# Kernel tuning notes

Hardware: AMD Instinct MI355X
Metric: run time of the kernel (lower is better)

## Reference

```python
import jax, jax.numpy as jnp
import numpy as np


def setup_inputs() -> dict:
    key = jax.random.key(0)
    k1, k2 = jax.random.split(key)
    N, P1, P2, D = 2, 16384, 16384, 3
    cloud1 = jax.random.normal(k1, (N, P1, D), dtype=jnp.float32)
    cloud2 = jax.random.normal(k2, (N, P2, D), dtype=jnp.float32)
    return {"cloud1": cloud1, "cloud2": cloud2}


def reference(cloud1, cloud2):
    # Chamfer distance (tensorflow_graphics convention):
    #   mean_i min_j ||a_i - b_j||^2 + mean_j min_i ||a_i - b_j||^2, per batch.
    # Compute squared distances via the Gram trick to avoid a (N,P1,P2,3) tensor.
    sq1 = jnp.sum(cloud1 * cloud1, axis=-1)              # (N, P1)
    sq2 = jnp.sum(cloud2 * cloud2, axis=-1)              # (N, P2)
    inner = jnp.einsum("npd,nqd->npq", cloud1, cloud2)   # (N, P1, P2)
    sqdist = sq1[:, :, None] + sq2[:, None, :] - 2.0 * inner
    sqdist = jnp.maximum(sqdist, 0.0)  # numerical floor
    min_a_to_b = jnp.min(sqdist, axis=2)  # (N, P1)
    min_b_to_a = jnp.min(sqdist, axis=1)  # (N, P2)
    return jnp.mean(min_a_to_b, axis=1) + jnp.mean(min_b_to_a, axis=1)  # (N,)
```

## Files before the change

kernel.cpp:

```cpp
#include <hip/hip_runtime.h>

#define NBATCH 2
#define NPTS   16384
#define TPTS   32
#define NTILES (NPTS / TPTS)
#define JCH    8
#define NT_PER (NTILES / JCH)
#define TG     (NPTS / 256)

typedef float f32x16 __attribute__((ext_vector_type(16)));
typedef short s16x8  __attribute__((ext_vector_type(8)));

__device__ __forceinline__ unsigned short f2bf(float f) {
    unsigned u = __float_as_uint(f);
    u += 0x7FFF + ((u >> 16) & 1);
    return (unsigned short)(u >> 16);
}
__device__ __forceinline__ float bf2f(unsigned short h) {
    return __uint_as_float((unsigned)h << 16);
}

__device__ __forceinline__ f32x16 mfma32(s16x8 a, s16x8 b) {
    f32x16 d;
    asm volatile("v_mfma_f32_32x32x16_bf16 %0, %1, %2, 0"
                 : "=&v"(d) : "v"(a), "v"(b));
    return d;
}
__device__ __forceinline__ void min3f(float& acc, float x, float y) {
    asm("v_min3_f32 %0, %1, %2, %3" : "=v"(acc) : "v"(acc), "v"(x), "v"(y));
}
__device__ __forceinline__ float min3v(float x, float y, float z) {
    float r;
    asm("v_min3_f32 %0, %1, %2, %3" : "=v"(r) : "v"(x), "v"(y), "v"(z));
    return r;
}

__global__ __launch_bounds__(256) void pack_panels(
    const float* __restrict__ c1, const float* __restrict__ c2,
    unsigned short* __restrict__ apan, unsigned short* __restrict__ bpan,
    unsigned int* __restrict__ mins)
{
    int tid = blockIdx.x * 256 + threadIdx.x;
    if (tid < 2 * NBATCH * NPTS) mins[tid] = 0x7F7F7F7Fu;

    int lane   = tid & 63;
    int tile   = (tid >> 6) & (NTILES - 1);
    int n      = (tid >> 15) & 1;
    int whichB = (tid >> 16) & 1;
    int wc     = (tid >> 17) & 1;

    const float* src = wc ? c2 : c1;

    int p = tile * TPTS + (lane & 31);
    const float* q = src + ((size_t)n * NPTS + p) * 3;
    float x = q[0], y = q[1], z = q[2];

    unsigned short xh = f2bf(x), yh = f2bf(y), zh = f2bf(z);
    unsigned short xl = f2bf(x - bf2f(xh)), yl = f2bf(y - bf2f(yh)), zl = f2bf(z - bf2f(zh));
    float sq = x * x + y * y + z * z;
    unsigned short sh = f2bf(sq);
    unsigned short sl = f2bf(sq - bf2f(sh));
    const unsigned short one = 0x3F80;

    unsigned short slots[16];
    if (!whichB) {
        slots[0]=xh;  slots[1]=yh;  slots[2]=zh;
        slots[3]=xl;  slots[4]=yl;  slots[5]=zl;
        slots[6]=xh;  slots[7]=yh;  slots[8]=zh;
        slots[9]=one; slots[10]=one;
        slots[11]=sh; slots[12]=sl;
        slots[13]=0;  slots[14]=0;  slots[15]=0;
    } else {
        unsigned short mxh=f2bf(-2.f*bf2f(xh)), myh=f2bf(-2.f*bf2f(yh)), mzh=f2bf(-2.f*bf2f(zh));
        unsigned short mxl=f2bf(-2.f*bf2f(xl)), myl=f2bf(-2.f*bf2f(yl)), mzl=f2bf(-2.f*bf2f(zl));
        slots[0]=mxh; slots[1]=myh; slots[2]=mzh;
        slots[3]=mxh; slots[4]=myh; slots[5]=mzh;
        slots[6]=mxl; slots[7]=myl; slots[8]=mzl;
        slots[9]=sh;  slots[10]=sl;
        slots[11]=one; slots[12]=one;
        slots[13]=0;  slots[14]=0;  slots[15]=0;
    }

    int j0 = (lane >> 5) * 8;
    uint4 w;
    w.x = (unsigned)slots[j0+0] | ((unsigned)slots[j0+1] << 16);
    w.y = (unsigned)slots[j0+2] | ((unsigned)slots[j0+3] << 16);
    w.z = (unsigned)slots[j0+4] | ((unsigned)slots[j0+5] << 16);
    w.w = (unsigned)slots[j0+6] | ((unsigned)slots[j0+7] << 16);
    unsigned short* pan = whichB ? bpan : apan;
    uint4* dst = (uint4*)pan + ((size_t)((wc * 2 + n) * NTILES + tile) * 64 + lane);
    *dst = w;
}

__global__ __launch_bounds__(256, 4) void chamfer_rows(
    const unsigned short* __restrict__ apan, const unsigned short* __restrict__ bpan,
    unsigned int* __restrict__ mins )
{
    __shared__ float ldsr[128 * 33];

    int bid = blockIdx.x;
    const int jc  = bid & (JCH - 1); bid >>= 3;
    const int tg  = bid & (TG - 1);  bid >>= 6;
    const int n   = bid & 1;         bid >>= 1;
    const int dir = bid;

    const int lane   = threadIdx.x & 63;
    const int wv     = threadIdx.x >> 6;
    const int colw   = lane & 31;
    const int laneHi = lane >> 5;
    const int rt0    = tg * 8 + wv * 2;

    const s16x8 a0 = *(const s16x8*)(
        apan + ((size_t)((dir * 2 + n) * NTILES + rt0) * 64 + lane) * 8);
    const s16x8 a1 = *(const s16x8*)(
        apan + ((size_t)((dir * 2 + n) * NTILES + rt0 + 1) * 64 + lane) * 8);
    const unsigned short* B =
        bpan + ((size_t)(((1 - dir) * 2 + n) * NTILES + jc * NT_PER) * 64 + lane) * 8;

#define LDT(t) (*(const s16x8*)(B + (size_t)(t) * 512))

    float rm0[16], rm1[16];
    #pragma unroll
    for (int r = 0; r < 16; ++r) { rm0[r] = 3.0e38f; rm1[r] = 3.0e38f; }

    s16x8 b0 = LDT(0), b1 = LDT(1), b2 = LDT(2), b3 = LDT(3);

#define PHASE(bc0, bc1, p0, p1)                                               \
    {                                                                         \
        f32x16 dA = mfma32(a0, bc0);                                          \
        f32x16 dB = mfma32(a0, bc1);                                          \
        __builtin_amdgcn_sched_barrier(0);                                    \
        asm volatile("s_nop 7\n\ts_nop 7\n\ts_nop 7" :: "v"(dA), "v"(dB));    \
        __builtin_amdgcn_sched_barrier(0);                                    \
        _Pragma("unroll")                                                     \
        for (int r = 0; r < 16; ++r) min3f(rm0[r], dA[r], dB[r]);             \
        f32x16 dC = mfma32(a1, bc0);                                          \
        f32x16 dD = mfma32(a1, bc1);                                          \
        bc0 = LDT((p0) & (NT_PER - 1));                                       \
        bc1 = LDT((p1) & (NT_PER - 1));                                       \
        __builtin_amdgcn_sched_barrier(0);                                    \
        asm volatile("s_nop 7\n\ts_nop 7\n\ts_nop 7" :: "v"(dC), "v"(dD));    \
        __builtin_amdgcn_sched_barrier(0);                                    \
        _Pragma("unroll")                                                     \
        for (int r = 0; r < 16; ++r) min3f(rm1[r], dC[r], dD[r]);             \
    }

    #pragma unroll
    for (int tt = 0; tt < NT_PER / 4; ++tt) {
        PHASE(b0, b1, 4 * tt + 4, 4 * tt + 5);
        PHASE(b2, b3, 4 * tt + 6, 4 * tt + 7);
    }
#undef PHASE
#undef LDT

    unsigned int* md = mins + (size_t)(dir * NBATCH + n) * NPTS + tg * 256;
    const int tid = threadIdx.x;

    #pragma unroll
    for (int p = 0; p < 2; ++p) {
        const float* rm = p ? rm1 : rm0;
        #pragma unroll
        for (int r = 0; r < 16; ++r) {
            const int cr = (r & 3) + 8 * (r >> 2) + 4 * laneHi;
            ldsr[(wv * 32 + cr) * 33 + colw] = rm[r];
        }
        __syncthreads();
        if (tid < 128) {
            const float* Lr = &ldsr[tid * 33];
            float c = min3v(Lr[0], Lr[1], Lr[2]);
            #pragma unroll
            for (int u = 0; u < 14; ++u) c = min3v(c, Lr[3 + 2 * u], Lr[4 + 2 * u]);
            c = fminf(c, Lr[31]);
            int rowg = (tid >> 5) * 64 + p * 32 + (tid & 31);
            atomicMin(&md[rowg], __float_as_uint(fmaxf(c, 0.0f)));
        }
        __syncthreads();
    }
}

__global__ __launch_bounds__(1024) void chamfer_out(
    const unsigned int* __restrict__ mins, float* __restrict__ out)
{
    int n = blockIdx.x;
    float acc = 0.0f;
    for (int i = threadIdx.x; i < NPTS; i += 1024) {
        acc += __uint_as_float(mins[(0 * NBATCH + n) * NPTS + i]);
        acc += __uint_as_float(mins[(1 * NBATCH + n) * NPTS + i]);
    }
    for (int off = 32; off > 0; off >>= 1) acc += __shfl_down(acc, off, 64);
    __shared__ float sm[16];
    int wv = threadIdx.x >> 6, ln = threadIdx.x & 63;
    if (ln == 0) sm[wv] = acc;
    __syncthreads();
    if (threadIdx.x == 0) {
        float tot = 0.0f;
        #pragma unroll
        for (int w = 0; w < 16; ++w) tot += sm[w];
        out[n] = tot / (float)NPTS;
    }
}

extern "C" void kernel_launch(void* const* d_in, const int* in_sizes, int n_in,
                              void* d_out, int out_size, void* d_ws, size_t ws_size,
                              hipStream_t stream)
{
    const float* c1 = (const float*)d_in[0];
    const float* c2 = (const float*)d_in[1];
    float* out = (float*)d_out;

    char* ws = (char*)d_ws;
    unsigned int*   mins = (unsigned int*)ws;
    unsigned short* apan = (unsigned short*)(ws + (size_t)(2 * NBATCH * NPTS) * 4);
    unsigned short* bpan = apan + (size_t)2 * NBATCH * NTILES * 512;

    pack_panels<<<(1 << 18) / 256, 256, 0, stream>>>(c1, c2, apan, bpan, mins);
    chamfer_rows<<<2 * NBATCH * TG * JCH, 256, 0, stream>>>(apan, bpan, mins);
    chamfer_out<<<NBATCH, 1024, 0, stream>>>(mins, out);
}
```

Before: 52.15 us.

## Stage B tiles through double-buffered LDS shared across waves

```diff
diff --git a/kernel.cpp b/kernel.cpp
--- a/kernel.cpp
+++ b/kernel.cpp
@@ -6,6 +6,7 @@
 #define NTILES (NPTS / TPTS)
 #define JCH    8
 #define NT_PER (NTILES / JCH)
+#define NQUAD  (NT_PER / 4)
 #define TG     (NPTS / 256)
 
 typedef float f32x16 __attribute__((ext_vector_type(16)));
@@ -97,6 +98,7 @@
     unsigned int* __restrict__ mins )
 {
     __shared__ float ldsr[128 * 33];
+    short* bst = (short*)ldsr;
 
     int bid = blockIdx.x;
     const int jc  = bid & (JCH - 1); bid >>= 3;
@@ -117,41 +119,49 @@
     const unsigned short* B =
         bpan + ((size_t)(((1 - dir) * 2 + n) * NTILES + jc * NT_PER) * 64 + lane) * 8;
 
-#define LDT(t) (*(const s16x8*)(B + (size_t)(t) * 512))
-
     float rm0[16], rm1[16];
     #pragma unroll
     for (int r = 0; r < 16; ++r) { rm0[r] = 3.0e38f; rm1[r] = 3.0e38f; }
 
-    s16x8 b0 = LDT(0), b1 = LDT(1), b2 = LDT(2), b3 = LDT(3);
-
-#define PHASE(bc0, bc1, p0, p1)                                               \
+#define DUOF(aa, rmv, tt0, tt1)                                               \
     {                                                                         \
-        f32x16 dA = mfma32(a0, bc0);                                          \
-        f32x16 dB = mfma32(a0, bc1);                                          \
+        f32x16 dX = mfma32(aa, tt0);                                          \
+        f32x16 dY = mfma32(aa, tt1);                                          \
         __builtin_amdgcn_sched_barrier(0);                                    \
-        asm volatile("s_nop 7\n\ts_nop 7\n\ts_nop 7" :: "v"(dA), "v"(dB));    \
+        asm volatile("s_nop 7\n\ts_nop 7\n\ts_nop 7" :: "v"(dX), "v"(dY));    \
         __builtin_amdgcn_sched_barrier(0);                                    \
         _Pragma("unroll")                                                     \
-        for (int r = 0; r < 16; ++r) min3f(rm0[r], dA[r], dB[r]);             \
-        f32x16 dC = mfma32(a1, bc0);                                          \
-        f32x16 dD = mfma32(a1, bc1);                                          \
-        bc0 = LDT((p0) & (NT_PER - 1));                                       \
-        bc1 = LDT((p1) & (NT_PER - 1));                                       \
-        __builtin_amdgcn_sched_barrier(0);                                    \
-        asm volatile("s_nop 7\n\ts_nop 7\n\ts_nop 7" :: "v"(dC), "v"(dD));    \
-        __builtin_amdgcn_sched_barrier(0);                                    \
-        _Pragma("unroll")                                                     \
-        for (int r = 0; r < 16; ++r) min3f(rm1[r], dC[r], dD[r]);             \
-    }
-
-    #pragma unroll
-    for (int tt = 0; tt < NT_PER / 4; ++tt) {
-        PHASE(b0, b1, 4 * tt + 4, 4 * tt + 5);
-        PHASE(b2, b3, 4 * tt + 6, 4 * tt + 7);
-    }
-#undef PHASE
-#undef LDT
+        for (int r = 0; r < 16; ++r) min3f(rmv[r], dX[r], dY[r]);             \
+    }
+
+    {
+        s16x8 g0 = *(const s16x8*)(B + (size_t)wv * 512);
+        *(s16x8*)(bst + wv * 512 + lane * 8) = g0;
+    }
+
+    #pragma unroll 2
+    for (int q = 0; q < NQUAD; ++q) {
+        const int b = q & 1;
+        __syncthreads();
+
+        const int nq = (q + 1) & (NQUAD - 1);
+        const s16x8 g = *(const s16x8*)(B + (size_t)(nq * 4 + wv) * 512);
+
+        const short* tb = bst + b * 2048 + lane * 8;
+        s16x8 t0 = *(const s16x8*)(tb);
+        s16x8 t1 = *(const s16x8*)(tb + 512);
+        s16x8 t2 = *(const s16x8*)(tb + 1024);
+        s16x8 t3 = *(const s16x8*)(tb + 1536);
+        DUOF(a0, rm0, t0, t1);
+        DUOF(a1, rm1, t0, t1);
+        DUOF(a0, rm0, t2, t3);
+        DUOF(a1, rm1, t2, t3);
+
+        *(s16x8*)(bst + (b ^ 1) * 2048 + wv * 512 + lane * 8) = g;
+    }
+#undef DUOF
+
+    __syncthreads();
 
     unsigned int* md = mins + (size_t)(dir * NBATCH + n) * NPTS + tg * 256;
     const int tid = threadIdx.x;
```

Result: faster. 50.55 us (-3.1%).

## Compute distance matrix once and reduce both row and column minima

Applied to the files above, without the earlier changes.

```diff
diff --git a/kernel.cpp b/kernel.cpp
--- a/kernel.cpp
+++ b/kernel.cpp
@@ -4,9 +4,9 @@
 #define NPTS   16384
 #define TPTS   32
 #define NTILES (NPTS / TPTS)
-#define JCH    8
+#define JCH    16
 #define NT_PER (NTILES / JCH)
-#define TG     (NPTS / 256)
+#define TG     (NPTS / 128)
 
 typedef float f32x16 __attribute__((ext_vector_type(16)));
 typedef short s16x8  __attribute__((ext_vector_type(8)));
@@ -19,6 +19,7 @@
 __device__ __forceinline__ float bf2f(unsigned short h) {
     return __uint_as_float((unsigned)h << 16);
 }
+__device__ __forceinline__ unsigned umin2(unsigned a, unsigned b) { return a < b ? a : b; }
 
 __device__ __forceinline__ f32x16 mfma32(s16x8 a, s16x8 b) {
     f32x16 d;
@@ -34,6 +35,13 @@
     asm("v_min3_f32 %0, %1, %2, %3" : "=v"(r) : "v"(x), "v"(y), "v"(z));
     return r;
 }
+__device__ __forceinline__ float tree16(const f32x16& d) {
+    float c = min3v(d[0], d[1], d[2]);
+    c = min3v(c, d[3],  d[4]);  c = min3v(c, d[5],  d[6]);
+    c = min3v(c, d[7],  d[8]);  c = min3v(c, d[9],  d[10]);
+    c = min3v(c, d[11], d[12]); c = min3v(c, d[13], d[14]);
+    return fminf(c, d[15]);
+}
 
 __global__ __launch_bounds__(256) void pack_panels(
     const float* __restrict__ c1, const float* __restrict__ c2,
@@ -47,9 +55,8 @@
     int tile   = (tid >> 6) & (NTILES - 1);
     int n      = (tid >> 15) & 1;
     int whichB = (tid >> 16) & 1;
-    int wc     = (tid >> 17) & 1;
-
-    const float* src = wc ? c2 : c1;
+
+    const float* src = whichB ? c2 : c1;
 
     int p = tile * TPTS + (lane & 31);
     const float* q = src + ((size_t)n * NPTS + p) * 3;
@@ -88,93 +95,96 @@
     w.z = (unsigned)slots[j0+4] | ((unsigned)slots[j0+5] << 16);
     w.w = (unsigned)slots[j0+6] | ((unsigned)slots[j0+7] << 16);
     unsigned short* pan = whichB ? bpan : apan;
-    uint4* dst = (uint4*)pan + ((size_t)((wc * 2 + n) * NTILES + tile) * 64 + lane);
+    uint4* dst = (uint4*)pan + ((size_t)(n * NTILES + tile) * 64 + lane);
     *dst = w;
 }
 
-__global__ __launch_bounds__(256, 4) void chamfer_rows(
+__global__ __launch_bounds__(256, 4) void chamfer_mm(
     const unsigned short* __restrict__ apan, const unsigned short* __restrict__ bpan,
-    unsigned int* __restrict__ mins )
+    unsigned int* __restrict__ rowmins, unsigned int* __restrict__ colmins)
 {
     __shared__ float ldsr[128 * 33];
+    unsigned int (*lcol)[NT_PER * 32] =
+        (unsigned int (*)[NT_PER * 32])ldsr;
 
     int bid = blockIdx.x;
-    const int jc  = bid & (JCH - 1); bid >>= 3;
-    const int tg  = bid & (TG - 1);  bid >>= 6;
-    const int n   = bid & 1;         bid >>= 1;
-    const int dir = bid;
+    const int jc = bid & (JCH - 1); bid >>= 4;
+    const int tg = bid & (TG - 1);  bid >>= 7;
+    const int n  = bid;
 
     const int lane   = threadIdx.x & 63;
     const int wv     = threadIdx.x >> 6;
     const int colw   = lane & 31;
     const int laneHi = lane >> 5;
-    const int rt0    = tg * 8 + wv * 2;
-
-    const s16x8 a0 = *(const s16x8*)(
-        apan + ((size_t)((dir * 2 + n) * NTILES + rt0) * 64 + lane) * 8);
-    const s16x8 a1 = *(const s16x8*)(
-        apan + ((size_t)((dir * 2 + n) * NTILES + rt0 + 1) * 64 + lane) * 8);
+    const int mt     = tg * 4 + wv;
+
+    const s16x8 a = *(const s16x8*)(
+        apan + ((size_t)(n * NTILES + mt) * 64 + lane) * 8);
     const unsigned short* B =
-        bpan + ((size_t)(((1 - dir) * 2 + n) * NTILES + jc * NT_PER) * 64 + lane) * 8;
+        bpan + ((size_t)(n * NTILES + jc * NT_PER) * 64 + lane) * 8;
 
 #define LDT(t) (*(const s16x8*)(B + (size_t)(t) * 512))
 
-    float rm0[16], rm1[16];
-    #pragma unroll
-    for (int r = 0; r < 16; ++r) { rm0[r] = 3.0e38f; rm1[r] = 3.0e38f; }
+    float rm[16];
+    #pragma unroll
+    for (int r = 0; r < 16; ++r) rm[r] = 3.0e38f;
 
     s16x8 b0 = LDT(0), b1 = LDT(1), b2 = LDT(2), b3 = LDT(3);
 
-#define PHASE(bc0, bc1, p0, p1)                                               \
+#define PHASE(bc0, bc1, t0, t1, p0, p1)                                       \
     {                                                                         \
-        f32x16 dA = mfma32(a0, bc0);                                          \
-        f32x16 dB = mfma32(a0, bc1);                                          \
-        __builtin_amdgcn_sched_barrier(0);                                    \
-        asm volatile("s_nop 7\n\ts_nop 7\n\ts_nop 7" :: "v"(dA), "v"(dB));    \
-        __builtin_amdgcn_sched_barrier(0);                                    \
-        _Pragma("unroll")                                                     \
-        for (int r = 0; r < 16; ++r) min3f(rm0[r], dA[r], dB[r]);             \
-        f32x16 dC = mfma32(a1, bc0);                                          \
-        f32x16 dD = mfma32(a1, bc1);                                          \
+        __builtin_amdgcn_s_setprio(1);                                        \
+        f32x16 dX = mfma32(a, bc0);                                           \
+        f32x16 dY = mfma32(a, bc1);                                           \
+        __builtin_amdgcn_s_setprio(0);                                        \
         bc0 = LDT((p0) & (NT_PER - 1));                                       \
         bc1 = LDT((p1) & (NT_PER - 1));                                       \
         __builtin_amdgcn_sched_barrier(0);                                    \
-        asm volatile("s_nop 7\n\ts_nop 7\n\ts_nop 7" :: "v"(dC), "v"(dD));    \
+        asm volatile("s_nop 7\n\ts_nop 7\n\ts_nop 7" :: "v"(dX), "v"(dY));    \
         __builtin_amdgcn_sched_barrier(0);                                    \
         _Pragma("unroll")                                                     \
-        for (int r = 0; r < 16; ++r) min3f(rm1[r], dC[r], dD[r]);             \
+        for (int r = 0; r < 16; ++r) min3f(rm[r], dX[r], dY[r]);              \
+        float c0 = tree16(dX), c1 = tree16(dY);                               \
+        c0 = fminf(c0, __shfl_xor(c0, 32, 64));                               \
+        c1 = fminf(c1, __shfl_xor(c1, 32, 64));                               \
+        lcol[wv][(t0) * 32 + colw] = __float_as_uint(fmaxf(c0, 0.f));         \
+        lcol[wv][(t1) * 32 + colw] = __float_as_uint(fmaxf(c1, 0.f));         \
     }
 
     #pragma unroll
     for (int tt = 0; tt < NT_PER / 4; ++tt) {
-        PHASE(b0, b1, 4 * tt + 4, 4 * tt + 5);
-        PHASE(b2, b3, 4 * tt + 6, 4 * tt + 7);
+        PHASE(b0, b1, 4 * tt,     4 * tt + 1, 4 * tt + 4, 4 * tt + 5);
+        PHASE(b2, b3, 4 * tt + 2, 4 * tt + 3, 4 * tt + 6, 4 * tt + 7);
     }
 #undef PHASE
 #undef LDT
 
-    unsigned int* md = mins + (size_t)(dir * NBATCH + n) * NPTS + tg * 256;
+    __syncthreads();
+    unsigned int* cbase = colmins + (size_t)n * NPTS + jc * (NT_PER * 32);
+    #pragma unroll
+    for (int u = 0; u < (NT_PER * 32) / 256; ++u) {
+        int s = u * 256 + threadIdx.x;
+        unsigned int k = umin2(umin2(lcol[0][s], lcol[1][s]),
+                               umin2(lcol[2][s], lcol[3][s]));
+        atomicMin(&cbase[s], k);
+    }
+    __syncthreads();
+
+    #pragma unroll
+    for (int r = 0; r < 16; ++r) {
+        const int cr = (r & 3) + 8 * (r >> 2) + 4 * laneHi;
+        ldsr[(wv * 32 + cr) * 33 + colw] = rm[r];
+    }
+    __syncthreads();
     const int tid = threadIdx.x;
-
-    #pragma unroll
-    for (int p = 0; p < 2; ++p) {
-        const float* rm = p ? rm1 : rm0;
+    if (tid < 128) {
+        const float* Lr = &ldsr[tid * 33];
+        float c = min3v(Lr[0], Lr[1], Lr[2]);
         #pragma unroll
-        for (int r = 0; r < 16; ++r) {
-            const int cr = (r & 3) + 8 * (r >> 2) + 4 * laneHi;
-            ldsr[(wv * 32 + cr) * 33 + colw] = rm[r];
-        }
-        __syncthreads();
-        if (tid < 128) {
-            const float* Lr = &ldsr[tid * 33];
-            float c = min3v(Lr[0], Lr[1], Lr[2]);
-            #pragma unroll
-            for (int u = 0; u < 14; ++u) c = min3v(c, Lr[3 + 2 * u], Lr[4 + 2 * u]);
-            c = fminf(c, Lr[31]);
-            int rowg = (tid >> 5) * 64 + p * 32 + (tid & 31);
-            atomicMin(&md[rowg], __float_as_uint(fmaxf(c, 0.0f)));
-        }
-        __syncthreads();
+        for (int u = 0; u < 14; ++u) c = min3v(c, Lr[3 + 2 * u], Lr[4 + 2 * u]);
+        c = fminf(c, Lr[31]);
+        atomicMin(&rowmins[(size_t)n * NPTS + tg * 128 + tid],
+                  __float_as_uint(fmaxf(c, 0.0f)));
     }
 }
 
@@ -211,9 +221,12 @@
     char* ws = (char*)d_ws;
     unsigned int*   mins = (unsigned int*)ws;
     unsigned short* apan = (unsigned short*)(ws + (size_t)(2 * NBATCH * NPTS) * 4);
-    unsigned short* bpan = apan + (size_t)2 * NBATCH * NTILES * 512;
-
-    pack_panels<<<(1 << 18) / 256, 256, 0, stream>>>(c1, c2, apan, bpan, mins);
-    chamfer_rows<<<2 * NBATCH * TG * JCH, 256, 0, stream>>>(apan, bpan, mins);
+    unsigned short* bpan = apan + (size_t)NBATCH * NTILES * 512;
+
+    unsigned int* rowmins = mins;
+    unsigned int* colmins = mins + (size_t)NBATCH * NPTS;
+
+    pack_panels<<<(1 << 17) / 256, 256, 0, stream>>>(c1, c2, apan, bpan, mins);
+    chamfer_mm<<<NBATCH * TG * JCH, 256, 0, stream>>>(apan, bpan, rowmins, colmins);
     chamfer_out<<<NBATCH, 1024, 0, stream>>>(mins, out);
 }
```

Measured after the change: 46.62 us. -10.6%, faster.
